# Kernel optimization log

Measured on AMD Instinct MI355X. Metric: run time of the kernel, lower is better.

Reference implementation:

```python
import jax, jax.numpy as jnp
import numpy as np

HIDDEN = 1024
B, S = 4, 2048

def setup_inputs() -> dict:
    key = jax.random.key(0)
    k1, k2 = jax.random.split(key)
    hidden_states = jax.random.normal(k1, (B, S, HIDDEN), dtype=jnp.float32)
    # torch nn.Linear weight layout: [out_features, in_features]
    W_proj = jax.random.normal(k2, (3 * HIDDEN, HIDDEN), dtype=jnp.float32) * (1.0 / np.sqrt(HIDDEN))
    b_proj = jnp.zeros((3 * HIDDEN,), dtype=jnp.float32)
    return {"hidden_states": hidden_states, "W_proj": W_proj, "b_proj": b_proj}

def reference(hidden_states, W_proj, b_proj):
    h = hidden_states.shape[-1]
    # fused QKV projection: y = x @ W^T + b
    qkv = jnp.einsum('bsh,oh->bso', hidden_states, W_proj) + b_proj
    q, k, v = jnp.split(qkv, 3, axis=-1)  # each [B,S,H]
    scale = 1.0 / jnp.sqrt(jnp.asarray(h, dtype=q.dtype))
    scores = jnp.einsum('bqh,bkh->bqk', q, k) * scale  # [B,S,S]
    attn = jax.nn.softmax(scores, axis=-1)
    out = jnp.einsum('bqk,bkh->bqh', attn, v)
    return out
```

## Files before the change

### kernel.cpp

```cpp
#include <hip/hip_runtime.h>
#include <stdint.h>

#define HIDDEN 1024
#define BATCH  4
#define SEQ    2048
#define TOKENS (BATCH * SEQ)
#define QKVD   (3 * HIDDEN)

typedef unsigned short u16;
typedef __attribute__((ext_vector_type(8))) short   short8;
typedef __attribute__((ext_vector_type(4))) float   floatx4;

__device__ __forceinline__ u16 f32_bf16_rne(float f) {
    unsigned int u = __float_as_uint(f);
    u += 0x7FFFu + ((u >> 16) & 1u);
    return (u16)(u >> 16);
}

__device__ __forceinline__ void gl16(const u16* g, u16* l) {
    __builtin_amdgcn_global_load_lds(
        (const __attribute__((address_space(1))) void*)g,
        (__attribute__((address_space(3))) void*)l, 16, 0, 0);
}

#define PBAR() do { __builtin_amdgcn_sched_barrier(0); \
    asm volatile("s_barrier" ::: "memory"); } while (0)
#define LG0() asm volatile("s_waitcnt lgkmcnt(0)" ::: "memory")
#define VM4() do { __builtin_amdgcn_sched_barrier(0); \
    asm volatile("s_waitcnt vmcnt(4)" ::: "memory"); } while (0)

__global__ __launch_bounds__(256) void cvt2_bf16_kernel(
        const float* __restrict__ sa, const float* __restrict__ sb,
        u16* __restrict__ da, u16* __restrict__ db, int n4a, int n4tot) {
    int i = blockIdx.x * 256 + threadIdx.x;
    if (i >= n4tot) return;
    float4 v;
    if (i < n4a) v = ((const float4*)sa)[i];
    else         v = ((const float4*)sb)[i - n4a];
    ushort4 o;
    o.x = f32_bf16_rne(v.x); o.y = f32_bf16_rne(v.y);
    o.z = f32_bf16_rne(v.z); o.w = f32_bf16_rne(v.w);
    if (i < n4a) ((ushort4*)da)[i] = o;
    else         ((ushort4*)db)[i - n4a] = o;
}

template <int EPI, int WM>
__global__ __launch_bounds__(512, 2) void gemm_bt(
        const u16* __restrict__ A, const u16* __restrict__ B,
        void* __restrict__ Cv, const float* __restrict__ bias,
        int K, int lda, int ldb, int ldc,
        size_t sA, size_t sB, size_t sC, float scale) {
    constexpr int BM    = 2 * WM;
    constexpr int MIH   = WM / 32;
    constexpr int ASLAB = BM * 64;
    constexpr int BSLAB = 256 * 64;
    constexpr int BUFB  = 2 * ASLAB + 2 * BSLAB;
    __shared__ __align__(16) char lds[2][BUFB];

    const int t    = threadIdx.x;
    const int lane = t & 63;
    const int wid  = t >> 6;
    const int wr   = wid >> 2;
    const int wc   = wid & 3;
    const int bm   = blockIdx.y * BM;
    const int bn   = blockIdx.x * 256;

    const u16* Ab = A + (size_t)blockIdx.z * sA;
    const u16* Bb = B + (size_t)blockIdx.z * sB;

    const int r0 = t >> 2;
    const int sl = (t & 3) ^ ((r0 >> 1) & 3);
    const u16* gA0 = Ab + (size_t)(bm + r0) * lda + sl * 8;
    const u16* gA1 = gA0 + (size_t)128 * lda;
    const u16* gB0 = Bb + (size_t)(bn + r0) * ldb + sl * 8;
    const u16* gB1 = gB0 + (size_t)128 * ldb;

    const int fr  = lane & 15;
    const int kc  = lane >> 4;
    const int frb = fr * 64 + ((kc ^ ((fr >> 1) & 3)) << 4);

    floatx4 acc[2 * MIH][4];
#pragma unroll
    for (int i = 0; i < 2 * MIH; i++)
#pragma unroll
        for (int j = 0; j < 4; j++) acc[i][j] = (floatx4){0.f, 0.f, 0.f, 0.f};

    short8 aF[MIH][2], bLo[2][2], bHi[2][2];

    auto rdA = [&](short8 (&dst)[MIH][2], const char* bp, int miBase) {
#pragma unroll
        for (int m = 0; m < MIH; m++)
#pragma unroll
            for (int ks = 0; ks < 2; ks++)
                dst[m][ks] = *(const short8*)(bp + ks * ASLAB +
                    (wr * WM + (miBase + m) * 16) * 64 + frb);
    };
    auto rdB = [&](short8 (&dst)[2][2], const char* bp, int niBase) {
#pragma unroll
        for (int n = 0; n < 2; n++)
#pragma unroll
            for (int ks = 0; ks < 2; ks++)
                dst[n][ks] = *(const short8*)(bp + 2 * ASLAB + ks * BSLAB +
                    (wc * 64 + (niBase + n) * 16) * 64 + frb);
    };
    auto mf = [&](short8 (&av)[MIH][2], short8 (&bv)[2][2], int miB, int niB) {
        __builtin_amdgcn_s_setprio(1);
#pragma unroll
        for (int m = 0; m < MIH; m++)
#pragma unroll
            for (int n = 0; n < 2; n++)
#pragma unroll
                for (int ks = 0; ks < 2; ks++)
                    acc[miB + m][niB + n] = __builtin_amdgcn_mfma_f32_16x16x32_bf16(
                        av[m][ks], bv[n][ks], acc[miB + m][niB + n], 0, 0, 0);
        __builtin_amdgcn_s_setprio(0);
    };

#define STA(buf, ks, sc) do { \
    char* d = &lds[buf][(ks) * ASLAB] + wid * 1024; \
    gl16(gA0 + (sc) + (ks) * 32, (u16*)d); \
    if constexpr (WM == 128) gl16(gA1 + (sc) + (ks) * 32, (u16*)(d + 8192)); \
  } while (0)
#define STB(buf, ks, sc) do { \
    char* d = &lds[buf][2 * ASLAB + (ks) * BSLAB] + wid * 1024; \
    gl16(gB0 + (sc) + (ks) * 32, (u16*)d); \
    gl16(gB1 + (sc) + (ks) * 32, (u16*)(d + 8192)); \
  } while (0)

#define GROUP(q, S1, S2, S3, S4) { \
    const char* bp = &lds[q][0]; \
    rdA(aF, bp, 0); rdB(bLo, bp, 0); S1; PBAR(); LG0(); \
    mf(aF, bLo, 0, 0);   PBAR(); \
    rdB(bHi, bp, 2);                S2; PBAR(); LG0(); \
    mf(aF, bHi, 0, 2);   PBAR(); \
    rdA(aF, bp, MIH);               S3; PBAR(); LG0(); \
    mf(aF, bHi, MIH, 2); PBAR(); \
    S4; VM4(); PBAR(); \
    mf(aF, bLo, MIH, 0); PBAR(); \
}

    STA(0, 0, 0); STA(0, 1, 0); STB(0, 0, 0); STB(0, 1, 0);
    STB(1, 0, 64); STB(1, 1, 64);
    VM4(); PBAR();

    const int nk = K >> 6;
    for (int T = 0; T < nk; T += 2) {
        const int c1 = (T + 1) << 6;
        const int c2 = (T + 2 < nk ? T + 2 : nk - 1) << 6;
        const int c3 = (T + 3 < nk ? T + 3 : nk - 1) << 6;
        GROUP(0, STA(1, 0, c1), STA(1, 1, c1), STB(0, 0, c2), STB(0, 1, c2))
        GROUP(1, STA(0, 0, c2), STA(0, 1, c2), STB(1, 0, c3), STB(1, 1, c3))
    }
    asm volatile("s_waitcnt vmcnt(0)" ::: "memory");

#undef GROUP
#undef STB
#undef STA

    const int crow0 = bm + wr * WM + kc * 4;
    const int ccol0 = bn + wc * 64 + fr;
    const size_t coff = (size_t)blockIdx.z * sC;

    if (EPI == 0) {
        u16* C = (u16*)Cv;
        float bv[4];
#pragma unroll
        for (int ni = 0; ni < 4; ni++) bv[ni] = bias[ccol0 + ni * 16];
#pragma unroll
        for (int mi = 0; mi < 2 * MIH; mi++)
#pragma unroll
            for (int ni = 0; ni < 4; ni++)
#pragma unroll
                for (int r = 0; r < 4; r++)
                    C[coff + (size_t)(crow0 + mi * 16 + r) * ldc + (ccol0 + ni * 16)] =
                        f32_bf16_rne(acc[mi][ni][r] + bv[ni]);
    } else {
        float* C = (float*)Cv;
#pragma unroll
        for (int mi = 0; mi < 2 * MIH; mi++)
#pragma unroll
            for (int ni = 0; ni < 4; ni++)
#pragma unroll
                for (int r = 0; r < 4; r++) {
                    float v = acc[mi][ni][r];
                    if (EPI == 1) v *= scale;
                    C[coff + (size_t)(crow0 + mi * 16 + r) * ldc + (ccol0 + ni * 16)] = v;
                }
    }
}

__global__ __launch_bounds__(256) void softmax_kernel(
        const float* __restrict__ S, u16* __restrict__ P) {
    __shared__ float redm[4];
    __shared__ float reds[4];
    const size_t base = (size_t)blockIdx.x * SEQ;
    const int t = threadIdx.x, lane = t & 63, wid = t >> 6;
    const float4* src = (const float4*)(S + base);
    float4 a = src[t], b = src[t + 256];

    float m = fmaxf(fmaxf(fmaxf(a.x, a.y), fmaxf(a.z, a.w)),
                    fmaxf(fmaxf(b.x, b.y), fmaxf(b.z, b.w)));
#pragma unroll
    for (int off = 32; off; off >>= 1) m = fmaxf(m, __shfl_xor(m, off, 64));
    if (lane == 0) redm[wid] = m;
    __syncthreads();
    m = fmaxf(fmaxf(redm[0], redm[1]), fmaxf(redm[2], redm[3]));

    float e[8];
    e[0] = __expf(a.x - m); e[1] = __expf(a.y - m);
    e[2] = __expf(a.z - m); e[3] = __expf(a.w - m);
    e[4] = __expf(b.x - m); e[5] = __expf(b.y - m);
    e[6] = __expf(b.z - m); e[7] = __expf(b.w - m);
    float s = e[0] + e[1] + e[2] + e[3] + e[4] + e[5] + e[6] + e[7];
#pragma unroll
    for (int off = 32; off; off >>= 1) s += __shfl_xor(s, off, 64);
    if (lane == 0) reds[wid] = s;
    __syncthreads();
    s = reds[0] + reds[1] + reds[2] + reds[3];
    const float r = 1.f / s;

    ushort4* dst = (ushort4*)(P + base);
    ushort4 o0, o1;
    o0.x = f32_bf16_rne(e[0] * r); o0.y = f32_bf16_rne(e[1] * r);
    o0.z = f32_bf16_rne(e[2] * r); o0.w = f32_bf16_rne(e[3] * r);
    o1.x = f32_bf16_rne(e[4] * r); o1.y = f32_bf16_rne(e[5] * r);
    o1.z = f32_bf16_rne(e[6] * r); o1.w = f32_bf16_rne(e[7] * r);
    dst[t] = o0;
    dst[t + 256] = o1;
}

__global__ __launch_bounds__(256) void transposeV_kernel(
        const u16* __restrict__ qkv, u16* __restrict__ Vt) {
    __shared__ u16 tile[64][66];
    const int b = blockIdx.z;
    const int s0 = blockIdx.x * 64, h0 = blockIdx.y * 64;
    const int t = threadIdx.x;
    const int c = t & 63, r4 = t >> 6;
#pragma unroll
    for (int i = 0; i < 16; i++) {
        int sl = i * 4 + r4;
        tile[sl][c] = qkv[(size_t)(b * SEQ + s0 + sl) * QKVD + 2 * HIDDEN + h0 + c];
    }
    __syncthreads();
#pragma unroll
    for (int i = 0; i < 16; i++) {
        int hl = i * 4 + r4;
        Vt[(size_t)(b * HIDDEN + h0 + hl) * SEQ + s0 + c] = tile[c][hl];
    }
}

extern "C" void kernel_launch(void* const* d_in, const int* in_sizes, int n_in,
                              void* d_out, int out_size, void* d_ws, size_t ws_size,
                              hipStream_t stream) {
    const float* x    = (const float*)d_in[0];
    const float* W    = (const float*)d_in[1];
    const float* bias = (const float*)d_in[2];
    float* out = (float*)d_out;

    u16* Xb  = (u16*)d_ws;
    u16* Wb  = Xb + (size_t)TOKENS * HIDDEN;
    u16* qkv = Wb + (size_t)QKVD * HIDDEN;
    float* scores = (float*)(qkv + (size_t)TOKENS * QKVD);
    u16* P  = (u16*)(scores + (size_t)BATCH * SEQ * SEQ);
    u16* Vt = P + (size_t)BATCH * SEQ * SEQ;

    {
        const int n4a = TOKENS * HIDDEN / 4;
        const int n4b = QKVD * HIDDEN / 4;
        const int n4t = n4a + n4b;
        cvt2_bf16_kernel<<<(n4t + 255) / 256, 256, 0, stream>>>(x, W, Xb, Wb, n4a, n4t);
    }

    gemm_bt<0, 128><<<dim3(QKVD / 256, TOKENS / 256, 1), 512, 0, stream>>>(
        Xb, Wb, qkv, bias, HIDDEN, HIDDEN, HIDDEN, QKVD, 0, 0, 0, 1.f);

    gemm_bt<1, 128><<<dim3(SEQ / 256, SEQ / 256, BATCH), 512, 0, stream>>>(
        qkv, qkv + HIDDEN, scores, nullptr, HIDDEN, QKVD, QKVD, SEQ,
        (size_t)SEQ * QKVD, (size_t)SEQ * QKVD, (size_t)SEQ * SEQ, 0.03125f);

    softmax_kernel<<<BATCH * SEQ, 256, 0, stream>>>(scores, P);

    transposeV_kernel<<<dim3(SEQ / 64, HIDDEN / 64, BATCH), 256, 0, stream>>>(qkv, Vt);

    gemm_bt<2, 64><<<dim3(HIDDEN / 256, SEQ / 128, BATCH), 512, 0, stream>>>(
        P, Vt, out, nullptr, SEQ, SEQ, SEQ, HIDDEN,
        (size_t)SEQ * SEQ, (size_t)HIDDEN * SEQ, (size_t)SEQ * HIDDEN, 1.f);
}
```

Before: 258.2 us.

## Restructure GEMM to 128-row tiles with register double-buffered fragment prefetch

Fixes the GEMM tile at 128x256 for all three matmuls, which halves the M tile for the QKV and score GEMMs, and rewrites the main loop. Each group now prefetches the next stage's A and B fragments from LDS into alternate register sets while MFMAs run. The explicit lgkmcnt waits are dropped so LDS reads overlap with compute. The smaller tiles give more blocks and better occupancy for the two large GEMMs, at the cost of more global reloads of B per output element.

```diff
diff --git a/kernel.cpp b/kernel.cpp
--- a/kernel.cpp
+++ b/kernel.cpp
@@ -25,7 +25,6 @@
 
 #define PBAR() do { __builtin_amdgcn_sched_barrier(0); \
     asm volatile("s_barrier" ::: "memory"); } while (0)
-#define LG0() asm volatile("s_waitcnt lgkmcnt(0)" ::: "memory")
 #define VM4() do { __builtin_amdgcn_sched_barrier(0); \
     asm volatile("s_waitcnt vmcnt(4)" ::: "memory"); } while (0)
 
@@ -44,15 +43,13 @@
     else         ((ushort4*)db)[i - n4a] = o;
 }
 
-template <int EPI, int WM>
+template <int EPI>
 __global__ __launch_bounds__(512, 2) void gemm_bt(
         const u16* __restrict__ A, const u16* __restrict__ B,
         void* __restrict__ Cv, const float* __restrict__ bias,
         int K, int lda, int ldb, int ldc,
         size_t sA, size_t sB, size_t sC, float scale) {
-    constexpr int BM    = 2 * WM;
-    constexpr int MIH   = WM / 32;
-    constexpr int ASLAB = BM * 64;
+    constexpr int ASLAB = 128 * 64;
     constexpr int BSLAB = 256 * 64;
     constexpr int BUFB  = 2 * ASLAB + 2 * BSLAB;
     __shared__ __align__(16) char lds[2][BUFB];
@@ -62,7 +59,7 @@
     const int wid  = t >> 6;
     const int wr   = wid >> 2;
     const int wc   = wid & 3;
-    const int bm   = blockIdx.y * BM;
+    const int bm   = blockIdx.y * 128;
     const int bn   = blockIdx.x * 256;
 
     const u16* Ab = A + (size_t)blockIdx.z * sA;
@@ -71,7 +68,6 @@
     const int r0 = t >> 2;
     const int sl = (t & 3) ^ ((r0 >> 1) & 3);
     const u16* gA0 = Ab + (size_t)(bm + r0) * lda + sl * 8;
-    const u16* gA1 = gA0 + (size_t)128 * lda;
     const u16* gB0 = Bb + (size_t)(bn + r0) * ldb + sl * 8;
     const u16* gB1 = gB0 + (size_t)128 * ldb;
 
@@ -79,21 +75,23 @@
     const int kc  = lane >> 4;
     const int frb = fr * 64 + ((kc ^ ((fr >> 1) & 3)) << 4);
 
-    floatx4 acc[2 * MIH][4];
-#pragma unroll
-    for (int i = 0; i < 2 * MIH; i++)
+    floatx4 acc[4][4];
+#pragma unroll
+    for (int i = 0; i < 4; i++)
 #pragma unroll
         for (int j = 0; j < 4; j++) acc[i][j] = (floatx4){0.f, 0.f, 0.f, 0.f};
 
-    short8 aF[MIH][2], bLo[2][2], bHi[2][2];
-
-    auto rdA = [&](short8 (&dst)[MIH][2], const char* bp, int miBase) {
-#pragma unroll
-        for (int m = 0; m < MIH; m++)
+    short8 aF0A[2][2], aF0B[2][2];
+    short8 bLoA[2][2], bLoB[2][2];
+    short8 aF1[2][2],  bHi[2][2];
+
+    auto rdA = [&](short8 (&dst)[2][2], const char* bp, int miBase) {
+#pragma unroll
+        for (int m = 0; m < 2; m++)
 #pragma unroll
             for (int ks = 0; ks < 2; ks++)
                 dst[m][ks] = *(const short8*)(bp + ks * ASLAB +
-                    (wr * WM + (miBase + m) * 16) * 64 + frb);
+                    (wr * 64 + (miBase + m) * 16) * 64 + frb);
     };
     auto rdB = [&](short8 (&dst)[2][2], const char* bp, int niBase) {
 #pragma unroll
@@ -103,10 +101,10 @@
                 dst[n][ks] = *(const short8*)(bp + 2 * ASLAB + ks * BSLAB +
                     (wc * 64 + (niBase + n) * 16) * 64 + frb);
     };
-    auto mf = [&](short8 (&av)[MIH][2], short8 (&bv)[2][2], int miB, int niB) {
+    auto mf8 = [&](short8 (&av)[2][2], short8 (&bv)[2][2], int miB, int niB) {
         __builtin_amdgcn_s_setprio(1);
 #pragma unroll
-        for (int m = 0; m < MIH; m++)
+        for (int m = 0; m < 2; m++)
 #pragma unroll
             for (int n = 0; n < 2; n++)
 #pragma unroll
@@ -116,40 +114,45 @@
         __builtin_amdgcn_s_setprio(0);
     };
 
-#define STA(buf, ks, sc) do { \
-    char* d = &lds[buf][(ks) * ASLAB] + wid * 1024; \
-    gl16(gA0 + (sc) + (ks) * 32, (u16*)d); \
-    if constexpr (WM == 128) gl16(gA1 + (sc) + (ks) * 32, (u16*)(d + 8192)); \
+#define STA(bq, sc) do { \
+    char* d = &lds[bq][0] + wid * 1024; \
+    gl16(gA0 + (sc),      (u16*)d); \
+    gl16(gA0 + (sc) + 32, (u16*)(d + ASLAB)); \
   } while (0)
-#define STB(buf, ks, sc) do { \
-    char* d = &lds[buf][2 * ASLAB + (ks) * BSLAB] + wid * 1024; \
-    gl16(gB0 + (sc) + (ks) * 32, (u16*)d); \
-    gl16(gB1 + (sc) + (ks) * 32, (u16*)(d + 8192)); \
+#define STB(bq, sc) do { \
+    char* d = &lds[bq][2 * ASLAB] + wid * 1024; \
+    gl16(gB0 + (sc),      (u16*)d); \
+    gl16(gB1 + (sc),      (u16*)(d + 8192)); \
+    gl16(gB0 + (sc) + 32, (u16*)(d + BSLAB)); \
+    gl16(gB1 + (sc) + 32, (u16*)(d + BSLAB + 8192)); \
   } while (0)
 
-#define GROUP(q, S1, S2, S3, S4) { \
-    const char* bp = &lds[q][0]; \
-    rdA(aF, bp, 0); rdB(bLo, bp, 0); S1; PBAR(); LG0(); \
-    mf(aF, bLo, 0, 0);   PBAR(); \
-    rdB(bHi, bp, 2);                S2; PBAR(); LG0(); \
-    mf(aF, bHi, 0, 2);   PBAR(); \
-    rdA(aF, bp, MIH);               S3; PBAR(); LG0(); \
-    mf(aF, bHi, MIH, 2); PBAR(); \
-    S4; VM4(); PBAR(); \
-    mf(aF, bLo, MIH, 0); PBAR(); \
-}
-
-    STA(0, 0, 0); STA(0, 1, 0); STB(0, 0, 0); STB(0, 1, 0);
-    STB(1, 0, 64); STB(1, 1, 64);
-    VM4(); PBAR();
+#define GROUP(q, AF0C, BLOC, AF0N, BLON, SCN) { \
+    const char* bp = lds[q]; \
+    const char* np = lds[q ^ 1]; \
+    rdB(bHi, bp, 2); \
+    mf8(AF0C, BLOC, 0, 0); PBAR(); \
+    rdA(aF1, bp, 2); \
+    mf8(AF0C, bHi, 0, 2); PBAR(); \
+    STB(q, SCN); \
+    mf8(aF1, bHi, 2, 2); VM4(); PBAR(); \
+    rdA(AF0N, np, 0); rdB(BLON, np, 0); STA(q, SCN); \
+    mf8(aF1, BLOC, 2, 0); PBAR(); \
+}
+
+    STA(0, 0); STB(0, 0);
+    STA(1, 64); STB(1, 64);
+    __builtin_amdgcn_sched_barrier(0);
+    asm volatile("s_waitcnt vmcnt(6)" ::: "memory");
+    PBAR();
+    rdA(aF0A, lds[0], 0); rdB(bLoA, lds[0], 0);
 
     const int nk = K >> 6;
     for (int T = 0; T < nk; T += 2) {
-        const int c1 = (T + 1) << 6;
-        const int c2 = (T + 2 < nk ? T + 2 : nk - 1) << 6;
-        const int c3 = (T + 3 < nk ? T + 3 : nk - 1) << 6;
-        GROUP(0, STA(1, 0, c1), STA(1, 1, c1), STB(0, 0, c2), STB(0, 1, c2))
-        GROUP(1, STA(0, 0, c2), STA(0, 1, c2), STB(1, 0, c3), STB(1, 1, c3))
+        const int sc2 = (T + 2 < nk ? T + 2 : nk - 1) << 6;
+        const int sc3 = (T + 3 < nk ? T + 3 : nk - 1) << 6;
+        GROUP(0, aF0A, bLoA, aF0B, bLoB, sc2)
+        GROUP(1, aF0B, bLoB, aF0A, bLoA, sc3)
     }
     asm volatile("s_waitcnt vmcnt(0)" ::: "memory");
 
@@ -157,7 +160,7 @@
 #undef STB
 #undef STA
 
-    const int crow0 = bm + wr * WM + kc * 4;
+    const int crow0 = bm + wr * 64 + kc * 4;
     const int ccol0 = bn + wc * 64 + fr;
     const size_t coff = (size_t)blockIdx.z * sC;
 
@@ -167,7 +170,7 @@
 #pragma unroll
         for (int ni = 0; ni < 4; ni++) bv[ni] = bias[ccol0 + ni * 16];
 #pragma unroll
-        for (int mi = 0; mi < 2 * MIH; mi++)
+        for (int mi = 0; mi < 4; mi++)
 #pragma unroll
             for (int ni = 0; ni < 4; ni++)
 #pragma unroll
@@ -177,7 +180,7 @@
     } else {
         float* C = (float*)Cv;
 #pragma unroll
-        for (int mi = 0; mi < 2 * MIH; mi++)
+        for (int mi = 0; mi < 4; mi++)
 #pragma unroll
             for (int ni = 0; ni < 4; ni++)
 #pragma unroll
@@ -271,10 +274,10 @@
         cvt2_bf16_kernel<<<(n4t + 255) / 256, 256, 0, stream>>>(x, W, Xb, Wb, n4a, n4t);
     }
 
-    gemm_bt<0, 128><<<dim3(QKVD / 256, TOKENS / 256, 1), 512, 0, stream>>>(
+    gemm_bt<0><<<dim3(QKVD / 256, TOKENS / 128, 1), 512, 0, stream>>>(
         Xb, Wb, qkv, bias, HIDDEN, HIDDEN, HIDDEN, QKVD, 0, 0, 0, 1.f);
 
-    gemm_bt<1, 128><<<dim3(SEQ / 256, SEQ / 256, BATCH), 512, 0, stream>>>(
+    gemm_bt<1><<<dim3(SEQ / 256, SEQ / 128, BATCH), 512, 0, stream>>>(
         qkv, qkv + HIDDEN, scores, nullptr, HIDDEN, QKVD, QKVD, SEQ,
         (size_t)SEQ * QKVD, (size_t)SEQ * QKVD, (size_t)SEQ * SEQ, 0.03125f);
 
@@ -282,7 +285,7 @@
 
     transposeV_kernel<<<dim3(SEQ / 64, HIDDEN / 64, BATCH), 256, 0, stream>>>(qkv, Vt);
 
-    gemm_bt<2, 64><<<dim3(HIDDEN / 256, SEQ / 128, BATCH), 512, 0, stream>>>(
+    gemm_bt<2><<<dim3(HIDDEN / 256, SEQ / 128, BATCH), 512, 0, stream>>>(
         P, Vt, out, nullptr, SEQ, SEQ, SEQ, HIDDEN,
         (size_t)SEQ * SEQ, (size_t)HIDDEN * SEQ, (size_t)SEQ * HIDDEN, 1.f);
 }
```

Result: slower. 269.4 us (+4.3%).

## Fuse V transpose into a dedicated QKV projection GEMM epilogue

Applied to the files above, without the earlier changes.

Adds a dedicated QKV projection GEMM with a 128x256 tile and a K-step of 32 per LDS slab, double-buffered with async global-to-LDS loads. For the V column blocks it stages the output tile in LDS and writes V already transposed, so the separate transpose kernel and its extra read and write of V go away. The generic GEMM loses its bias/bf16 epilogue path. The new tile shape and pipeline change occupancy and scheduling for the projection, and the LDS-staged transpose adds a sync and strided LDS reads.

```diff
diff --git a/kernel.cpp b/kernel.cpp
--- a/kernel.cpp
+++ b/kernel.cpp
@@ -9,6 +9,7 @@
 
 typedef unsigned short u16;
 typedef __attribute__((ext_vector_type(8))) short   short8;
+typedef __attribute__((ext_vector_type(8))) unsigned short ushort8;
 typedef __attribute__((ext_vector_type(4))) float   floatx4;
 
 __device__ __forceinline__ u16 f32_bf16_rne(float f) {
@@ -23,6 +24,8 @@
         (__attribute__((address_space(3))) void*)l, 16, 0, 0);
 }
 
+#define SYNC3() do { __builtin_amdgcn_sched_barrier(0); \
+    asm volatile("s_waitcnt vmcnt(3)\n\ts_barrier" ::: "memory"); } while (0)
 #define PBAR() do { __builtin_amdgcn_sched_barrier(0); \
     asm volatile("s_barrier" ::: "memory"); } while (0)
 #define LG0() asm volatile("s_waitcnt lgkmcnt(0)" ::: "memory")
@@ -44,6 +47,157 @@
     else         ((ushort4*)db)[i - n4a] = o;
 }
 
+__global__ __launch_bounds__(512, 2) void gemm_qkv(
+        const u16* __restrict__ A, const u16* __restrict__ B,
+        u16* __restrict__ C, u16* __restrict__ Vt,
+        const float* __restrict__ bias) {
+    __shared__ __align__(16) u16 lds[2][2][(128 + 256) * 32];
+
+    const int t    = threadIdx.x;
+    const int lane = t & 63;
+    const int wid  = t >> 6;
+    const int wr   = wid >> 2;
+    const int wc   = wid & 3;
+    const int bm   = blockIdx.y * 128;
+    const int bn   = blockIdx.x * 256;
+
+    const int rA  = t >> 2;
+    const int sl  = (t & 3) ^ ((rA >> 1) & 3);
+    const u16* gA  = A + (size_t)(bm + rA) * 1024 + sl * 8;
+    const u16* gB0 = B + (size_t)(bn + rA) * 1024 + sl * 8;
+    const u16* gB1 = gB0 + (size_t)128 * 1024;
+
+    const int fr = lane & 15;
+    const int kc = lane >> 4;
+    const int fo = ((kc ^ ((fr >> 1) & 3)) << 4);
+    const int aoffB = (wr * 64 + fr) * 64 + fo;
+    const int boffB = (wc * 64 + fr) * 64 + fo;
+
+    floatx4 acc[4][4];
+#pragma unroll
+    for (int i = 0; i < 4; i++)
+#pragma unroll
+        for (int j = 0; j < 4; j++) acc[i][j] = (floatx4){0.f, 0.f, 0.f, 0.f};
+
+    short8 bfr0, bfr1, bfr2, bfr3, va0, va1;
+
+#define LDB4(BASE) \
+    bfr0 = *(const short8*)((BASE) + boffB);        \
+    bfr1 = *(const short8*)((BASE) + boffB + 1024); \
+    bfr2 = *(const short8*)((BASE) + boffB + 2048); \
+    bfr3 = *(const short8*)((BASE) + boffB + 3072);
+
+#define MFMA2(MI, A0, A1) \
+    __builtin_amdgcn_s_setprio(1); \
+    acc[MI][0]     = __builtin_amdgcn_mfma_f32_16x16x32_bf16(A0, bfr0, acc[MI][0], 0, 0, 0); \
+    acc[MI][1]     = __builtin_amdgcn_mfma_f32_16x16x32_bf16(A0, bfr1, acc[MI][1], 0, 0, 0); \
+    acc[MI][2]     = __builtin_amdgcn_mfma_f32_16x16x32_bf16(A0, bfr2, acc[MI][2], 0, 0, 0); \
+    acc[MI][3]     = __builtin_amdgcn_mfma_f32_16x16x32_bf16(A0, bfr3, acc[MI][3], 0, 0, 0); \
+    acc[(MI)+1][0] = __builtin_amdgcn_mfma_f32_16x16x32_bf16(A1, bfr0, acc[(MI)+1][0], 0, 0, 0); \
+    acc[(MI)+1][1] = __builtin_amdgcn_mfma_f32_16x16x32_bf16(A1, bfr1, acc[(MI)+1][1], 0, 0, 0); \
+    acc[(MI)+1][2] = __builtin_amdgcn_mfma_f32_16x16x32_bf16(A1, bfr2, acc[(MI)+1][2], 0, 0, 0); \
+    acc[(MI)+1][3] = __builtin_amdgcn_mfma_f32_16x16x32_bf16(A1, bfr3, acc[(MI)+1][3], 0, 0, 0); \
+    __builtin_amdgcn_s_setprio(0);
+
+#define ITER(BUF, SBUF, SCOL) { \
+    const char* As0_ = (const char*)&lds[BUF][0][0]; \
+    const char* Bs0_ = As0_ + 8192; \
+    const char* As1_ = (const char*)&lds[BUF][1][0]; \
+    const char* Bs1_ = As1_ + 8192; \
+    gl16(gA + (SCOL),       (u16*)((char*)&lds[SBUF][0][0]    + wid * 1024)); \
+    LDB4(Bs0_); \
+    va0 = *(const short8*)(As0_ + aoffB); \
+    va1 = *(const short8*)(As0_ + aoffB + 1024); \
+    MFMA2(0, va0, va1); \
+    gl16(gB0 + (SCOL),      (u16*)((char*)&lds[SBUF][0][4096] + wid * 1024)); \
+    gl16(gB1 + (SCOL),      (u16*)((char*)&lds[SBUF][0][8192] + wid * 1024)); \
+    va0 = *(const short8*)(As0_ + aoffB + 2048); \
+    va1 = *(const short8*)(As0_ + aoffB + 3072); \
+    MFMA2(2, va0, va1); \
+    SYNC3(); \
+    gl16(gA + (SCOL) + 32,  (u16*)((char*)&lds[SBUF][1][0]    + wid * 1024)); \
+    LDB4(Bs1_); \
+    va0 = *(const short8*)(As1_ + aoffB); \
+    va1 = *(const short8*)(As1_ + aoffB + 1024); \
+    MFMA2(0, va0, va1); \
+    gl16(gB0 + (SCOL) + 32, (u16*)((char*)&lds[SBUF][1][4096] + wid * 1024)); \
+    gl16(gB1 + (SCOL) + 32, (u16*)((char*)&lds[SBUF][1][8192] + wid * 1024)); \
+    va0 = *(const short8*)(As1_ + aoffB + 2048); \
+    va1 = *(const short8*)(As1_ + aoffB + 3072); \
+    MFMA2(2, va0, va1); \
+    SYNC3(); }
+
+    gl16(gA,       (u16*)((char*)&lds[0][0][0]    + wid * 1024));
+    gl16(gB0,      (u16*)((char*)&lds[0][0][4096] + wid * 1024));
+    gl16(gB1,      (u16*)((char*)&lds[0][0][8192] + wid * 1024));
+    gl16(gA + 32,  (u16*)((char*)&lds[0][1][0]    + wid * 1024));
+    gl16(gB0 + 32, (u16*)((char*)&lds[0][1][4096] + wid * 1024));
+    gl16(gB1 + 32, (u16*)((char*)&lds[0][1][8192] + wid * 1024));
+    SYNC3();
+
+    const int nk = 1024 >> 6;
+    for (int kt = 0; kt < nk; kt += 2) {
+        const int c1 = (kt + 1) << 6;
+        const int c2 = (kt + 2 < nk ? (kt + 2) : (nk - 1)) << 6;
+        ITER(0, 1, c1)
+        ITER(1, 0, c2)
+    }
+    asm volatile("s_waitcnt vmcnt(0)" ::: "memory");
+
+#undef ITER
+#undef MFMA2
+#undef LDB4
+
+    const int crow0 = bm + wr * 64 + kc * 4;
+    const int ccol0 = bn + wc * 64 + fr;
+    float bv[4];
+#pragma unroll
+    for (int ni = 0; ni < 4; ni++) bv[ni] = bias[ccol0 + ni * 16];
+
+    if (blockIdx.x < 8) {
+#pragma unroll
+        for (int mi = 0; mi < 4; mi++)
+#pragma unroll
+            for (int ni = 0; ni < 4; ni++)
+#pragma unroll
+                for (int r = 0; r < 4; r++)
+                    C[(size_t)(crow0 + mi * 16 + r) * QKVD + (ccol0 + ni * 16)] =
+                        f32_bf16_rne(acc[mi][ni][r] + bv[ni]);
+    } else {
+        __syncthreads();
+        u16 (*TB)[258] = (u16(*)[258]) & lds[0][0][0];
+        const int lr0 = wr * 64 + kc * 4;
+        const int lc0 = wc * 64 + fr;
+#pragma unroll
+        for (int mi = 0; mi < 4; mi++)
+#pragma unroll
+            for (int ni = 0; ni < 4; ni++)
+#pragma unroll
+                for (int r = 0; r < 4; r++)
+                    TB[lr0 + mi * 16 + r][lc0 + ni * 16] =
+                        f32_bf16_rne(acc[mi][ni][r] + bv[ni]);
+        __syncthreads();
+        const int b  = bm >> 11;
+        const int sb = bm & 2047;
+        const int h0 = bn - 2048;
+        for (int it = 0; it < 2; ++it) {
+            const int task = it * 512 + t;
+            const int h    = task & 255;
+            const int s0   = (task >> 8) * 32;
+            ushort8 v[4];
+#pragma unroll
+            for (int j8 = 0; j8 < 4; ++j8)
+#pragma unroll
+                for (int j = 0; j < 8; ++j)
+                    v[j8][j] = TB[s0 + j8 * 8 + j][h];
+            u16* dst = Vt + (size_t)(b * 1024 + h0 + h) * 2048 + sb + s0;
+#pragma unroll
+            for (int j8 = 0; j8 < 4; ++j8)
+                *(ushort8*)(dst + j8 * 8) = v[j8];
+        }
+    }
+}
+
 template <int EPI, int WM>
 __global__ __launch_bounds__(512, 2) void gemm_bt(
         const u16* __restrict__ A, const u16* __restrict__ B,
@@ -161,32 +315,17 @@
     const int ccol0 = bn + wc * 64 + fr;
     const size_t coff = (size_t)blockIdx.z * sC;
 
-    if (EPI == 0) {
-        u16* C = (u16*)Cv;
-        float bv[4];
-#pragma unroll
-        for (int ni = 0; ni < 4; ni++) bv[ni] = bias[ccol0 + ni * 16];
-#pragma unroll
-        for (int mi = 0; mi < 2 * MIH; mi++)
-#pragma unroll
-            for (int ni = 0; ni < 4; ni++)
-#pragma unroll
-                for (int r = 0; r < 4; r++)
-                    C[coff + (size_t)(crow0 + mi * 16 + r) * ldc + (ccol0 + ni * 16)] =
-                        f32_bf16_rne(acc[mi][ni][r] + bv[ni]);
-    } else {
-        float* C = (float*)Cv;
-#pragma unroll
-        for (int mi = 0; mi < 2 * MIH; mi++)
-#pragma unroll
-            for (int ni = 0; ni < 4; ni++)
-#pragma unroll
-                for (int r = 0; r < 4; r++) {
-                    float v = acc[mi][ni][r];
-                    if (EPI == 1) v *= scale;
-                    C[coff + (size_t)(crow0 + mi * 16 + r) * ldc + (ccol0 + ni * 16)] = v;
-                }
-    }
+    float* C = (float*)Cv;
+#pragma unroll
+    for (int mi = 0; mi < 2 * MIH; mi++)
+#pragma unroll
+        for (int ni = 0; ni < 4; ni++)
+#pragma unroll
+            for (int r = 0; r < 4; r++) {
+                float v = acc[mi][ni][r];
+                if (EPI == 1) v *= scale;
+                C[coff + (size_t)(crow0 + mi * 16 + r) * ldc + (ccol0 + ni * 16)] = v;
+            }
 }
 
 __global__ __launch_bounds__(256) void softmax_kernel(
@@ -229,26 +368,6 @@
     dst[t + 256] = o1;
 }
 
-__global__ __launch_bounds__(256) void transposeV_kernel(
-        const u16* __restrict__ qkv, u16* __restrict__ Vt) {
-    __shared__ u16 tile[64][66];
-    const int b = blockIdx.z;
-    const int s0 = blockIdx.x * 64, h0 = blockIdx.y * 64;
-    const int t = threadIdx.x;
-    const int c = t & 63, r4 = t >> 6;
-#pragma unroll
-    for (int i = 0; i < 16; i++) {
-        int sl = i * 4 + r4;
-        tile[sl][c] = qkv[(size_t)(b * SEQ + s0 + sl) * QKVD + 2 * HIDDEN + h0 + c];
-    }
-    __syncthreads();
-#pragma unroll
-    for (int i = 0; i < 16; i++) {
-        int hl = i * 4 + r4;
-        Vt[(size_t)(b * HIDDEN + h0 + hl) * SEQ + s0 + c] = tile[c][hl];
-    }
-}
-
 extern "C" void kernel_launch(void* const* d_in, const int* in_sizes, int n_in,
                               void* d_out, int out_size, void* d_ws, size_t ws_size,
                               hipStream_t stream) {
@@ -271,8 +390,8 @@
         cvt2_bf16_kernel<<<(n4t + 255) / 256, 256, 0, stream>>>(x, W, Xb, Wb, n4a, n4t);
     }
 
-    gemm_bt<0, 128><<<dim3(QKVD / 256, TOKENS / 256, 1), 512, 0, stream>>>(
-        Xb, Wb, qkv, bias, HIDDEN, HIDDEN, HIDDEN, QKVD, 0, 0, 0, 1.f);
+    gemm_qkv<<<dim3(QKVD / 256, TOKENS / 128, 1), 512, 0, stream>>>(
+        Xb, Wb, qkv, Vt, bias);
 
     gemm_bt<1, 128><<<dim3(SEQ / 256, SEQ / 256, BATCH), 512, 0, stream>>>(
         qkv, qkv + HIDDEN, scores, nullptr, HIDDEN, QKVD, QKVD, SEQ,
@@ -280,8 +399,6 @@
 
     softmax_kernel<<<BATCH * SEQ, 256, 0, stream>>>(scores, P);
 
-    transposeV_kernel<<<dim3(SEQ / 64, HIDDEN / 64, BATCH), 256, 0, stream>>>(qkv, Vt);
-
     gemm_bt<2, 64><<<dim3(HIDDEN / 256, SEQ / 128, BATCH), 512, 0, stream>>>(
         P, Vt, out, nullptr, SEQ, SEQ, SEQ, HIDDEN,
         (size_t)SEQ * SEQ, (size_t)HIDDEN * SEQ, (size_t)SEQ * HIDDEN, 1.f);
```

Result: no change. 259.3 us (+0.4%).
